# Performance work log

Measured on AMD Instinct MI355X. Metric: run time of the kernel, lower is better.

Reference implementation:

```python
import jax, jax.numpy as jnp
import numpy as np
from functools import partial

QLEVELS = 255.0  # 8-bit quantization
IN_MIN, IN_MAX = -0.45, 3.55

def quantize(x, mn, mx):
    # 8-bit uniform fake-quant with straight-through estimator (matches typical QAT Quantize)
    scale = (mx - mn) / QLEVELS
    q = jnp.round((jnp.clip(x, mn, mx) - mn) / scale) * scale + mn
    return x + jax.lax.stop_gradient(q - x)

def qweight(W):
    # per-tensor weight fake-quant (QLinear / QParallelDFRCell weight path)
    mn = jax.lax.stop_gradient(W.min())
    mx = jax.lax.stop_gradient(W.max())
    return quantize(W, mn, mx)

def setup_inputs() -> dict:
    key = jax.random.key(0)
    ks = jax.random.split(key, 8)
    B, H, D, P, Q = 8192, 128, 6, 196, 49
    x = jax.random.normal(ks[0], (B, P), dtype=jnp.float32)
    cell_out = jnp.zeros((D, B, H), dtype=jnp.float32)
    p1_W = jax.random.normal(ks[1], (Q, P), dtype=jnp.float32) * 0.05
    p1_b = jnp.zeros((Q,), dtype=jnp.float32)
    W0 = jax.random.normal(ks[2], (H, 1), dtype=jnp.float32) * 0.5
    a0 = jnp.asarray(0.5, dtype=jnp.float32)
    Wd = jax.random.normal(ks[3], (D - 1, H, H), dtype=jnp.float32) * (1.0 / np.sqrt(H))
    ad = jnp.full((D - 1,), 0.5, dtype=jnp.float32)
    fc1_W = jax.random.normal(ks[4], (8, H), dtype=jnp.float32) * (1.0 / np.sqrt(H))
    fc2_W = jax.random.normal(ks[5], (10, 8), dtype=jnp.float32) * 0.3
    fc2_b = jnp.zeros((10,), dtype=jnp.float32)
    return {"x": x, "cell_out": cell_out, "W0": W0, "a0": a0, "Wd": Wd, "ad": ad,
            "p1_W": p1_W, "p1_b": p1_b, "fc1_W": fc1_W, "fc2_W": fc2_W, "fc2_b": fc2_b}

def reference(x, cell_out, W0, a0, Wd, ad, p1_W, p1_b, fc1_W, fc2_W, fc2_b):
    # input quantization + QLinear fc_p1: [B,196] -> [B,49]
    xq = quantize(x, IN_MIN, IN_MAX)
    pix = xq @ qweight(p1_W).T + p1_b          # [B, 49]
    W0q = qweight(W0)                           # [H, 1]
    Wdq = jax.vmap(qweight)(Wd)                 # [5, H, H]
    n_deep = Wd.shape[0]

    pixels = pix.T[:, :, None]                  # [49, B, 1] scan sequence

    def step(carry, px):
        h0, hs = carry                          # h0: [B,H], hs: [5,B,H]
        h0 = jnp.tanh(px @ W0q.T + a0 * h0)     # QParallelDFRCell(1 -> H)
        prev = h0
        new_hs = []
        for i in range(n_deep):                 # QParallelDFRCell(H -> H), fixed small chain
            hi = jnp.tanh(prev @ Wdq[i].T + ad[i] * hs[i])
            new_hs.append(hi)
            prev = hi
        return (h0, jnp.stack(new_hs)), None

    (h0, hs), _ = jax.lax.scan(step, (cell_out[0], cell_out[1:]), pixels)
    last = hs[-1]                               # [B, H]
    out = jax.nn.relu(last @ qweight(fc1_W).T)  # QLinear(H->8, no bias) + ReLU
    out = out @ fc2_W.T + fc2_b                 # Linear(8->10)
    return out
```

## Files before the change

### kernel.cpp

```cpp
#include <hip/hip_runtime.h>
#include <hip/hip_fp16.h>

typedef __attribute__((ext_vector_type(8))) _Float16 half8;
typedef __attribute__((ext_vector_type(4))) _Float16 half4;
typedef __attribute__((ext_vector_type(4))) float f32x4;

#define B_TOT 8192
#define HDIM  128
#define NDEEP 5
#define PDIM  196
#define QDIM  49
#define BM    16
#define NPHASE (QDIM + NDEEP)

__device__ __forceinline__ float tanh_fast(float v) {
    float e = __builtin_amdgcn_exp2f(v * 2.885390082f);
    float r = __builtin_amdgcn_rcpf(e + 1.0f);
    return fmaf(-2.0f, r, 1.0f);
}

__device__ __forceinline__ float fquant(float v, float mn, float sc) {
    return rintf((v - mn) / sc) * sc + mn;
}

__global__ __launch_bounds__(256, 2) void dfr_all(
    const float* __restrict__ x,    const float* __restrict__ cell_out,
    const float* __restrict__ W0,   const float* __restrict__ a0p,
    const float* __restrict__ Wd,   const float* __restrict__ adp,
    const float* __restrict__ p1W,  const float* __restrict__ p1b,
    const float* __restrict__ fc1W, const float* __restrict__ fc2W,
    const float* __restrict__ fc2b, float* __restrict__ out)
{
    __shared__ __align__(16) char smem[4096 + 10 * 4096];
    float* pix  = (float*)smem;
    char*  actp = smem + 4096;

    const int tid  = threadIdx.x;
    const int lane = tid & 63;
    const int w    = tid >> 6;
    const int l15  = lane & 15;
    const int l4   = lane >> 4;
    const int r0   = blockIdx.x * BM;

    float* sred = (float*)smem;

    float qmn[8], qsc[8];
    {
        const float* srcs[8] = { p1W, W0, fc1W, Wd, Wd + HDIM*HDIM, Wd + 2*HDIM*HDIM,
                                 Wd + 3*HDIM*HDIM, Wd + 4*HDIM*HDIM };
        const int    ns[8]   = { QDIM*PDIM, HDIM, 8*HDIM, HDIM*HDIM, HDIM*HDIM,
                                 HDIM*HDIM, HDIM*HDIM, HDIM*HDIM };
#pragma unroll
        for (int s = 0; s < 8; s++) {
            const float* p = srcs[s]; const int n = ns[s];
            float mn = 1e30f, mx = -1e30f;
            for (int i = tid; i < n; i += 256) { float v = p[i]; mn = fminf(mn, v); mx = fmaxf(mx, v); }
            for (int off = 32; off; off >>= 1) {
                mn = fminf(mn, __shfl_down(mn, off));
                mx = fmaxf(mx, __shfl_down(mx, off));
            }
            if (lane == 0) { sred[w] = mn; sred[4 + w] = mx; }
            __syncthreads();
            mn = fminf(fminf(sred[0], sred[1]), fminf(sred[2], sred[3]));
            mx = fmaxf(fmaxf(sred[4], sred[5]), fmaxf(sred[6], sred[7]));
            __syncthreads();
            qmn[s] = mn; qsc[s] = (mx - mn) / 255.0f;
        }
    }

    half8 bw[NDEEP][2][4];
#pragma unroll
    for (int i = 0; i < NDEEP; i++) {
        const float mn = qmn[3 + i], sc = qsc[3 + i];
#pragma unroll
        for (int nt = 0; nt < 2; nt++)
#pragma unroll
            for (int kc = 0; kc < 4; kc++) {
                const float* src = Wd + (size_t)i * HDIM * HDIM
                                 + (size_t)(w * 32 + nt * 16 + l15) * HDIM + kc * 32 + l4 * 8;
                half8 h;
#pragma unroll
                for (int j = 0; j < 8; j++) h[j] = (_Float16)fquant(src[j], mn, sc);
                bw[i][nt][kc] = h;
            }
    }

    const float a0 = a0p[0];
    float adv[NDEEP];
#pragma unroll
    for (int i = 0; i < NDEEP; i++) adv[i] = adp[i];

    const int hr  = tid >> 4;
    const int hc0 = (tid & 15) * 8;
    float w0v[8], h0v[8];
#pragma unroll
    for (int j = 0; j < 8; j++) {
        w0v[j] = fquant(W0[hc0 + j], qmn[1], qsc[1]);
        h0v[j] = cell_out[(size_t)(r0 + hr) * HDIM + hc0 + j];
    }

    f32x4 st[NDEEP][2];
#pragma unroll
    for (int i = 0; i < NDEEP; i++)
#pragma unroll
        for (int nt = 0; nt < 2; nt++)
            st[i][nt] = *(const f32x4*)(cell_out + (size_t)(1 + i) * B_TOT * HDIM
                                 + (size_t)(r0 + l15) * HDIM + w * 32 + nt * 16 + l4 * 4);

    {
        _Float16* pq = (_Float16*)actp;
        _Float16* xq = (_Float16*)(actp + 28672);
        for (int idx = tid; idx < 16 * 224; idx += 256) {
            int r = idx / 224, p = idx - r * 224;
            float v = 0.0f;
            if (p < PDIM) {
                v = x[(size_t)(r0 + r) * PDIM + p];
                v = fminf(fmaxf(v, -0.45f), 3.55f);
                const float sc = 4.0f / 255.0f;
                v = rintf((v + 0.45f) / sc) * sc - 0.45f;
            }
            xq[idx] = (_Float16)v;
        }
        {
            const float mn = qmn[0], sc = qsc[0];
            for (int idx = tid; idx < 64 * 224; idx += 256) {
                int q = idx / 224, p = idx - q * 224;
                float v = 0.0f;
                if (q < QDIM && p < PDIM) v = fquant(p1W[q * PDIM + p], mn, sc);
                pq[idx] = (_Float16)v;
            }
        }
        __syncthreads();
        f32x4 accp = {0.f, 0.f, 0.f, 0.f};
#pragma unroll
        for (int kc = 0; kc < 7; kc++) {
            half8 aF = *(const half8*)(pq + (w * 16 + l15) * 224 + kc * 32 + l4 * 8);
            half8 bF = *(const half8*)(xq + l15 * 224 + kc * 32 + l4 * 8);
            accp = __builtin_amdgcn_mfma_f32_16x16x32_f16(aF, bF, accp, 0, 0, 0);
        }
#pragma unroll
        for (int j = 0; j < 4; j++) {
            int qj = w * 16 + l4 * 4 + j;
            accp[j] += (qj < QDIM) ? p1b[qj] : 0.0f;
        }
        *(f32x4*)(pix + l15 * 64 + w * 16 + l4 * 4) = accp;
        __syncthreads();
    }

    const int aswz  = (l15 & 7) << 4;
    int boff[4];
#pragma unroll
    for (int kc = 0; kc < 4; kc++) boff[kc] = l15 * 256 + ((kc * 64 + l4 * 16) ^ aswz);
    const int cb0   = w * 64 + l4 * 8;
    const int woff0 = l15 * 256 + (cb0 ^ aswz);
    const int woff1 = l15 * 256 + ((cb0 + 32) ^ aswz);
    const int h0off = hr * 256 + ((hc0 * 2) ^ ((hr & 7) << 4));
    const float* pixr = pix + hr * 64;

#define PHASE(P, SW, SR)                                                              \
    do {                                                                              \
        if ((P) < QDIM) {                                                             \
            float px = pixr[(P)];                                                     \
            half8 hh;                                                                 \
            _Pragma("unroll") for (int j = 0; j < 8; j++) {                           \
                float v = tanh_fast(fmaf(px, w0v[j], a0 * h0v[j]));                   \
                h0v[j] = v; hh[j] = (_Float16)v;                                      \
            }                                                                         \
            *(half8*)(actp + (SW) * 4096 + h0off) = hh;                               \
        }                                                                             \
        _Pragma("unroll") for (int i = 0; i < NDEEP; i++) {                           \
            int t_ = (P) - 1 - i;                                                     \
            if (t_ >= 0 && t_ < QDIM) {                                               \
                f32x4 acc0 = st[i][0] * adv[i];                                       \
                f32x4 acc1 = st[i][1] * adv[i];                                       \
                _Pragma("unroll") for (int kc = 0; kc < 4; kc++) {                    \
                    half8 b_ = *(const half8*)(actp + i * 8192 + (SR) * 4096 + boff[kc]); \
                    acc0 = __builtin_amdgcn_mfma_f32_16x16x32_f16(bw[i][0][kc], b_, acc0, 0, 0, 0); \
                    acc1 = __builtin_amdgcn_mfma_f32_16x16x32_f16(bw[i][1][kc], b_, acc1, 0, 0, 0); \
                }                                                                     \
                half4 hA, hB;                                                         \
                _Pragma("unroll") for (int j = 0; j < 4; j++) {                       \
                    acc0[j] = tanh_fast(acc0[j]);                                     \
                    acc1[j] = tanh_fast(acc1[j]);                                     \
                    hA[j] = (_Float16)acc0[j]; hB[j] = (_Float16)acc1[j];             \
                }                                                                     \
                st[i][0] = acc0; st[i][1] = acc1;                                     \
                if (i < NDEEP - 1) {                                                  \
                    *(half4*)(actp + (i + 1) * 8192 + (SW) * 4096 + woff0) = hA;      \
                    *(half4*)(actp + (i + 1) * 8192 + (SW) * 4096 + woff1) = hB;      \
                }                                                                     \
            }                                                                         \
        }                                                                             \
        __syncthreads();                                                              \
    } while (0)

#pragma unroll 1
    for (int p = 0; p < NPHASE; p += 2) {
        PHASE(p,     0, 1);
        PHASE(p + 1, 1, 0);
    }
#undef PHASE

    float* hs4 = (float*)actp;
    *(f32x4*)(hs4 + l15 * 136 + w * 32 + l4 * 4)      = st[NDEEP - 1][0];
    *(f32x4*)(hs4 + l15 * 136 + w * 32 + 16 + l4 * 4) = st[NDEEP - 1][1];
    __syncthreads();

    float* tmp = pix;
    if (tid < 128) {
        int r = tid >> 3, jj = tid & 7;
        const float* hrow = hs4 + r * 136;
        const float* fw   = fc1W + jj * HDIM;
        const float mn = qmn[2], sc = qsc[2];
        float acc = 0.f;
#pragma unroll 4
        for (int p = 0; p < HDIM; p++) acc += hrow[p] * fquant(fw[p], mn, sc);
        tmp[r * 8 + jj] = fmaxf(acc, 0.f);
    }
    __syncthreads();
    if (tid < 160) {
        int r = tid / 10, o = tid - r * 10;
        float acc = fc2b[o];
#pragma unroll
        for (int jj = 0; jj < 8; jj++) acc += tmp[r * 8 + jj] * fc2W[o * 8 + jj];
        out[(size_t)(r0 + r) * 10 + o] = acc;
    }
}

extern "C" void kernel_launch(void* const* d_in, const int* in_sizes, int n_in,
                              void* d_out, int out_size, void* d_ws, size_t ws_size,
                              hipStream_t stream)
{
    const float* x    = (const float*)d_in[0];
    const float* cell = (const float*)d_in[1];
    const float* W0   = (const float*)d_in[2];
    const float* a0   = (const float*)d_in[3];
    const float* Wd   = (const float*)d_in[4];
    const float* ad   = (const float*)d_in[5];
    const float* p1W  = (const float*)d_in[6];
    const float* p1b  = (const float*)d_in[7];
    const float* fc1  = (const float*)d_in[8];
    const float* fc2W = (const float*)d_in[9];
    const float* fc2b = (const float*)d_in[10];

    dfr_all<<<512, 256, 0, stream>>>(x, cell, W0, a0, Wd, ad, p1W, p1b,
                                     fc1, fc2W, fc2b, (float*)d_out);
}
```

Before: 361.3 us.

## Process 32 batch rows per block with 8 waves splitting hidden dimension

Doubles the rows per block to 32 and the block size to 512 threads. Each of the 8 waves now owns 16 output hidden columns across two 16-row batch tiles, instead of 32 columns for one tile. This halves the weight registers per wave and halves the grid to 256 blocks. The aim is to cut register pressure and redundant per-block weight quantization, at the cost of fewer blocks and larger per-phase barriers across 8 waves.

```diff
diff --git a/kernel.cpp b/kernel.cpp
--- a/kernel.cpp
+++ b/kernel.cpp
@@ -10,7 +10,7 @@
 #define NDEEP 5
 #define PDIM  196
 #define QDIM  49
-#define BM    16
+#define BM    32
 #define NPHASE (QDIM + NDEEP)
 
 __device__ __forceinline__ float tanh_fast(float v) {
@@ -23,7 +23,7 @@
     return rintf((v - mn) / sc) * sc + mn;
 }
 
-__global__ __launch_bounds__(256, 2) void dfr_all(
+__global__ __launch_bounds__(512) void dfr_all(
     const float* __restrict__ x,    const float* __restrict__ cell_out,
     const float* __restrict__ W0,   const float* __restrict__ a0p,
     const float* __restrict__ Wd,   const float* __restrict__ adp,
@@ -31,9 +31,9 @@
     const float* __restrict__ fc1W, const float* __restrict__ fc2W,
     const float* __restrict__ fc2b, float* __restrict__ out)
 {
-    __shared__ __align__(16) char smem[4096 + 10 * 4096];
+    __shared__ __align__(16) char smem[8192 + 10 * 8192];
     float* pix  = (float*)smem;
-    char*  actp = smem + 4096;
+    char*  actp = smem + 8192;
 
     const int tid  = threadIdx.x;
     const int lane = tid & 63;
@@ -54,35 +54,35 @@
         for (int s = 0; s < 8; s++) {
             const float* p = srcs[s]; const int n = ns[s];
             float mn = 1e30f, mx = -1e30f;
-            for (int i = tid; i < n; i += 256) { float v = p[i]; mn = fminf(mn, v); mx = fmaxf(mx, v); }
+            for (int i = tid; i < n; i += 512) { float v = p[i]; mn = fminf(mn, v); mx = fmaxf(mx, v); }
             for (int off = 32; off; off >>= 1) {
                 mn = fminf(mn, __shfl_down(mn, off));
                 mx = fmaxf(mx, __shfl_down(mx, off));
             }
-            if (lane == 0) { sred[w] = mn; sred[4 + w] = mx; }
+            if (lane == 0) { sred[w] = mn; sred[8 + w] = mx; }
             __syncthreads();
-            mn = fminf(fminf(sred[0], sred[1]), fminf(sred[2], sred[3]));
-            mx = fmaxf(fmaxf(sred[4], sred[5]), fmaxf(sred[6], sred[7]));
+            mn = fminf(fminf(fminf(sred[0], sred[1]), fminf(sred[2], sred[3])),
+                       fminf(fminf(sred[4], sred[5]), fminf(sred[6], sred[7])));
+            mx = fmaxf(fmaxf(fmaxf(sred[8], sred[9]), fmaxf(sred[10], sred[11])),
+                       fmaxf(fmaxf(sred[12], sred[13]), fmaxf(sred[14], sred[15])));
             __syncthreads();
             qmn[s] = mn; qsc[s] = (mx - mn) / 255.0f;
         }
     }
 
-    half8 bw[NDEEP][2][4];
+    half8 bw[NDEEP][4];
 #pragma unroll
     for (int i = 0; i < NDEEP; i++) {
         const float mn = qmn[3 + i], sc = qsc[3 + i];
 #pragma unroll
-        for (int nt = 0; nt < 2; nt++)
-#pragma unroll
-            for (int kc = 0; kc < 4; kc++) {
-                const float* src = Wd + (size_t)i * HDIM * HDIM
-                                 + (size_t)(w * 32 + nt * 16 + l15) * HDIM + kc * 32 + l4 * 8;
-                half8 h;
-#pragma unroll
-                for (int j = 0; j < 8; j++) h[j] = (_Float16)fquant(src[j], mn, sc);
-                bw[i][nt][kc] = h;
-            }
+        for (int kc = 0; kc < 4; kc++) {
+            const float* src = Wd + (size_t)i * HDIM * HDIM
+                             + (size_t)(w * 16 + l15) * HDIM + kc * 32 + l4 * 8;
+            half8 h;
+#pragma unroll
+            for (int j = 0; j < 8; j++) h[j] = (_Float16)fquant(src[j], mn, sc);
+            bw[i][kc] = h;
+        }
     }
 
     const float a0 = a0p[0];
@@ -103,14 +103,14 @@
 #pragma unroll
     for (int i = 0; i < NDEEP; i++)
 #pragma unroll
-        for (int nt = 0; nt < 2; nt++)
-            st[i][nt] = *(const f32x4*)(cell_out + (size_t)(1 + i) * B_TOT * HDIM
-                                 + (size_t)(r0 + l15) * HDIM + w * 32 + nt * 16 + l4 * 4);
+        for (int bt = 0; bt < 2; bt++)
+            st[i][bt] = *(const f32x4*)(cell_out + (size_t)(1 + i) * B_TOT * HDIM
+                                 + (size_t)(r0 + bt * 16 + l15) * HDIM + w * 16 + l4 * 4);
 
     {
         _Float16* pq = (_Float16*)actp;
         _Float16* xq = (_Float16*)(actp + 28672);
-        for (int idx = tid; idx < 16 * 224; idx += 256) {
+        for (int idx = tid; idx < 32 * 224; idx += 512) {
             int r = idx / 224, p = idx - r * 224;
             float v = 0.0f;
             if (p < PDIM) {
@@ -123,7 +123,7 @@
         }
         {
             const float mn = qmn[0], sc = qsc[0];
-            for (int idx = tid; idx < 64 * 224; idx += 256) {
+            for (int idx = tid; idx < 64 * 224; idx += 512) {
                 int q = idx / 224, p = idx - q * 224;
                 float v = 0.0f;
                 if (q < QDIM && p < PDIM) v = fquant(p1W[q * PDIM + p], mn, sc);
@@ -131,29 +131,33 @@
             }
         }
         __syncthreads();
+        const int qt = w & 3, bt = w >> 2;
         f32x4 accp = {0.f, 0.f, 0.f, 0.f};
 #pragma unroll
         for (int kc = 0; kc < 7; kc++) {
-            half8 aF = *(const half8*)(pq + (w * 16 + l15) * 224 + kc * 32 + l4 * 8);
-            half8 bF = *(const half8*)(xq + l15 * 224 + kc * 32 + l4 * 8);
+            half8 aF = *(const half8*)(pq + (qt * 16 + l15) * 224 + kc * 32 + l4 * 8);
+            half8 bF = *(const half8*)(xq + (bt * 16 + l15) * 224 + kc * 32 + l4 * 8);
             accp = __builtin_amdgcn_mfma_f32_16x16x32_f16(aF, bF, accp, 0, 0, 0);
         }
 #pragma unroll
         for (int j = 0; j < 4; j++) {
-            int qj = w * 16 + l4 * 4 + j;
+            int qj = qt * 16 + l4 * 4 + j;
             accp[j] += (qj < QDIM) ? p1b[qj] : 0.0f;
         }
-        *(f32x4*)(pix + l15 * 64 + w * 16 + l4 * 4) = accp;
+        *(f32x4*)(pix + (bt * 16 + l15) * 64 + qt * 16 + l4 * 4) = accp;
         __syncthreads();
     }
 
-    const int aswz  = (l15 & 7) << 4;
-    int boff[4];
-#pragma unroll
-    for (int kc = 0; kc < 4; kc++) boff[kc] = l15 * 256 + ((kc * 64 + l4 * 16) ^ aswz);
-    const int cb0   = w * 64 + l4 * 8;
-    const int woff0 = l15 * 256 + (cb0 ^ aswz);
-    const int woff1 = l15 * 256 + ((cb0 + 32) ^ aswz);
+    const int aswz = (l15 & 7) << 4;
+    int boff[2][4];
+#pragma unroll
+    for (int bt = 0; bt < 2; bt++)
+#pragma unroll
+        for (int kc = 0; kc < 4; kc++)
+            boff[bt][kc] = (bt * 16 + l15) * 256 + ((kc * 64 + l4 * 16) ^ aswz);
+    const int cb = w * 32 + l4 * 8;
+    const int woff0 = l15 * 256 + (cb ^ aswz);
+    const int woff1 = (16 + l15) * 256 + (cb ^ aswz);
     const int h0off = hr * 256 + ((hc0 * 2) ^ ((hr & 7) << 4));
     const float* pixr = pix + hr * 64;
 
@@ -166,17 +170,19 @@
                 float v = tanh_fast(fmaf(px, w0v[j], a0 * h0v[j]));                   \
                 h0v[j] = v; hh[j] = (_Float16)v;                                      \
             }                                                                         \
-            *(half8*)(actp + (SW) * 4096 + h0off) = hh;                               \
+            *(half8*)(actp + (SW) * 8192 + h0off) = hh;                               \
         }                                                                             \
         _Pragma("unroll") for (int i = 0; i < NDEEP; i++) {                           \
             int t_ = (P) - 1 - i;                                                     \
             if (t_ >= 0 && t_ < QDIM) {                                               \
                 f32x4 acc0 = st[i][0] * adv[i];                                       \
                 f32x4 acc1 = st[i][1] * adv[i];                                       \
+                const char* rbase = actp + i * 16384 + (SR) * 8192;                   \
                 _Pragma("unroll") for (int kc = 0; kc < 4; kc++) {                    \
-                    half8 b_ = *(const half8*)(actp + i * 8192 + (SR) * 4096 + boff[kc]); \
-                    acc0 = __builtin_amdgcn_mfma_f32_16x16x32_f16(bw[i][0][kc], b_, acc0, 0, 0, 0); \
-                    acc1 = __builtin_amdgcn_mfma_f32_16x16x32_f16(bw[i][1][kc], b_, acc1, 0, 0, 0); \
+                    half8 b0 = *(const half8*)(rbase + boff[0][kc]);                  \
+                    half8 b1 = *(const half8*)(rbase + boff[1][kc]);                  \
+                    acc0 = __builtin_amdgcn_mfma_f32_16x16x32_f16(bw[i][kc], b0, acc0, 0, 0, 0); \
+                    acc1 = __builtin_amdgcn_mfma_f32_16x16x32_f16(bw[i][kc], b1, acc1, 0, 0, 0); \
                 }                                                                     \
                 half4 hA, hB;                                                         \
                 _Pragma("unroll") for (int j = 0; j < 4; j++) {                       \
@@ -186,8 +192,9 @@
                 }                                                                     \
                 st[i][0] = acc0; st[i][1] = acc1;                                     \
                 if (i < NDEEP - 1) {                                                  \
-                    *(half4*)(actp + (i + 1) * 8192 + (SW) * 4096 + woff0) = hA;      \
-                    *(half4*)(actp + (i + 1) * 8192 + (SW) * 4096 + woff1) = hB;      \
+                    char* wb = actp + (i + 1) * 16384 + (SW) * 8192;                  \
+                    *(half4*)(wb + woff0) = hA;                                       \
+                    *(half4*)(wb + woff1) = hB;                                       \
                 }                                                                     \
             }                                                                         \
         }                                                                             \
@@ -202,12 +209,12 @@
 #undef PHASE
 
     float* hs4 = (float*)actp;
-    *(f32x4*)(hs4 + l15 * 136 + w * 32 + l4 * 4)      = st[NDEEP - 1][0];
-    *(f32x4*)(hs4 + l15 * 136 + w * 32 + 16 + l4 * 4) = st[NDEEP - 1][1];
+    *(f32x4*)(hs4 + (l15)      * 136 + w * 16 + l4 * 4) = st[NDEEP - 1][0];
+    *(f32x4*)(hs4 + (16 + l15) * 136 + w * 16 + l4 * 4) = st[NDEEP - 1][1];
     __syncthreads();
 
     float* tmp = pix;
-    if (tid < 128) {
+    if (tid < 256) {
         int r = tid >> 3, jj = tid & 7;
         const float* hrow = hs4 + r * 136;
         const float* fw   = fc1W + jj * HDIM;
@@ -218,7 +225,7 @@
         tmp[r * 8 + jj] = fmaxf(acc, 0.f);
     }
     __syncthreads();
-    if (tid < 160) {
+    if (tid < 320) {
         int r = tid / 10, o = tid - r * 10;
         float acc = fc2b[o];
 #pragma unroll
@@ -243,6 +250,6 @@
     const float* fc2W = (const float*)d_in[9];
     const float* fc2b = (const float*)d_in[10];
 
-    dfr_all<<<512, 256, 0, stream>>>(x, cell, W0, a0, Wd, ad, p1W, p1b,
+    dfr_all<<<256, 512, 0, stream>>>(x, cell, W0, a0, Wd, ad, p1W, p1b,
                                      fc1, fc2W, fc2b, (float*)d_out);
 }
```

After: 290.5 us. 1.24x faster.
